# Kernel tuning notes

Measured on AMD Instinct MI355X. Metric: run time of the kernel, lower is better.

## Reference

```python
import jax, jax.numpy as jnp
import numpy as np

NG, NC = 4096, 4096
FIN_G, FIN_C, D = 512, 512, 256
ALPHA = 0.2
NEG = -9.0e15

def leaky(x):
    return jnp.where(x >= 0, x, ALPHA * x)

def setup_inputs() -> dict:
    key = jax.random.key(0)
    ks = jax.random.split(key, 16)
    gene_x = jax.random.normal(ks[0], (NG, FIN_G), jnp.float32)
    cell_x = jax.random.normal(ks[1], (NC, FIN_C), jnp.float32)
    gene_adj = (jax.random.uniform(ks[2], (NG, NG)) < 0.05).astype(jnp.float32)
    gene_adj = jnp.maximum(gene_adj, jnp.eye(NG, dtype=jnp.float32))
    cell_adj = (jax.random.uniform(ks[3], (NC, NC)) < 0.05).astype(jnp.float32)
    cell_adj = jnp.maximum(cell_adj, jnp.eye(NC, dtype=jnp.float32))
    gene_cell_adj = (jax.random.uniform(ks[4], (NG, NC)) < 0.05).astype(jnp.float32)
    s = 1.414 * np.sqrt(6.0)
    def xav(k, shape):
        lim = s / np.sqrt(shape[0] + shape[1])
        return jax.random.uniform(k, shape, jnp.float32, -lim, lim)
    Wg = xav(ks[5], (D, FIN_G))
    Wc = xav(ks[6], (D, FIN_C))
    a_gg = xav(ks[7], (2 * D, 1))
    a_gc = xav(ks[8], (2 * D, 1))
    a_cc = xav(ks[9], (2 * D, 1))
    a_cg = xav(ks[10], (2 * D, 1))
    gate_g_w = xav(ks[11], (1, D))
    gate_c_w = xav(ks[12], (1, D))
    gate_g_b = jnp.full((1,), -2.0, jnp.float32)
    gate_c_b = jnp.full((1,), -2.0, jnp.float32)
    return dict(gene_x=gene_x, cell_x=cell_x, gene_adj=gene_adj, cell_adj=cell_adj,
                gene_cell_adj=gene_cell_adj, Wg=Wg, Wc=Wc, a_gg=a_gg, a_gc=a_gc,
                a_cc=a_cc, a_cg=a_cg, gate_g_w=gate_g_w, gate_g_b=gate_g_b,
                gate_c_w=gate_c_w, gate_c_b=gate_c_b)

def _gat_block(src_h, dst_h, a, adj):
    # attention of src rows over dst columns; adj: [Ns, Nd]
    d = src_h.shape[1]
    s1 = src_h @ a[:d, :]          # [Ns,1]
    s2 = dst_h @ a[d:, :]          # [Nd,1]
    e = leaky(s1 + s2.T)           # [Ns,Nd]
    att = jax.nn.softmax(jnp.where(adj > 0, e, NEG), axis=1)
    return att @ dst_h             # [Ns,d]

def reference(gene_x, cell_x, gene_adj, cell_adj, gene_cell_adj,
              Wg, Wc, a_gg, a_gc, a_cc, a_cg,
              gate_g_w, gate_g_b, gate_c_w, gate_c_b):
    gene_h = gene_x @ Wg.T   # [Ng,D]
    cell_h = cell_x @ Wc.T   # [Nc,D]
    gene_from_gene = _gat_block(gene_h, gene_h, a_gg, gene_adj)
    gene_from_cell = _gat_block(gene_h, cell_h, a_gc, gene_cell_adj)
    cell_from_cell = _gat_block(cell_h, cell_h, a_cc, cell_adj)
    cell_from_gene = _gat_block(cell_h, gene_h, a_cg, gene_cell_adj.T)
    gamma_g = jax.nn.sigmoid(gene_h @ gate_g_w.T + gate_g_b)  # [Ng,1]
    gamma_c = jax.nn.sigmoid(cell_h @ gate_c_w.T + gate_c_b)  # [Nc,1]
    gene_out = leaky(gene_h + gene_from_gene + gamma_g * gene_from_cell)
    cell_out = leaky(cell_h + cell_from_cell + gamma_c * cell_from_gene)
    return gene_out, cell_out
```

## Files before the change

kernel.cpp:

```cpp
#include <hip/hip_runtime.h>
#include <stdint.h>

#define NGC 4096
#define FIN 512
#define DD  256

typedef __attribute__((ext_vector_type(8))) short short8;
typedef __attribute__((ext_vector_type(4))) float f32x4;
typedef unsigned short u16;
typedef unsigned int   u32;
typedef unsigned long long u64;

static __device__ __forceinline__ float bf2f(u16 u){ return __uint_as_float(((u32)u)<<16); }
static __device__ __forceinline__ u16 f2bf(float f){
  u32 u = __float_as_uint(f);
  u += 0x7fffu + ((u>>16)&1u);
  return (u16)(u>>16);
}
static __device__ __forceinline__ float lk(float x){ return fmaxf(x, 0.2f*x); }
static __device__ __forceinline__ u64 shfl_xor64(u64 x, int m){
  u32 lo = (u32)x, hi = (u32)(x >> 32);
  lo = __shfl_xor(lo, m); hi = __shfl_xor(hi, m);
  return ((u64)hi << 32) | lo;
}

__global__ __launch_bounds__(256) void k_wcvt(
    const float* __restrict__ Wg, const float* __restrict__ Wc,
    u16* __restrict__ Wgbf, u16* __restrict__ Wcbf)
{
  int base = (blockIdx.x*256 + threadIdx.x)*4;
  float4 a = *(const float4*)(Wg + base);
  float4 b = *(const float4*)(Wc + base);
  ushort4 oa, ob;
  oa.x=f2bf(a.x); oa.y=f2bf(a.y); oa.z=f2bf(a.z); oa.w=f2bf(a.w);
  ob.x=f2bf(b.x); ob.y=f2bf(b.y); ob.z=f2bf(b.z); ob.w=f2bf(b.w);
  *(ushort4*)(Wgbf + base) = oa;
  *(ushort4*)(Wcbf + base) = ob;
}

__global__ __launch_bounds__(256) void k_pack(
    const float* __restrict__ gene_adj, const float* __restrict__ cell_adj,
    const float* __restrict__ gc_adj,   u64* __restrict__ packbits)
{
  int t = threadIdx.x, wid = t>>6, lane = t&63;
  int gw = blockIdx.x*4 + wid;
  int mat = gw >> 12;
  int row = gw & 4095;
  const float* src = (mat==0) ? gene_adj : (mat==1) ? cell_adj : gc_adj;
  const float* rp = src + (size_t)row*NGC;

  u64 myword = 0;
  #pragma unroll
  for(int i = 0; i < 16; i++){
    float4 v = *(const float4*)(rp + i*256 + lane*4);
    u32 nib = (v.x!=0.f?1u:0u) | (v.y!=0.f?2u:0u) | (v.z!=0.f?4u:0u) | (v.w!=0.f?8u:0u);
    u32 b  = nib | (__shfl_xor((int)nib, 1) << 4);
    u32 h  = b   | (__shfl_xor((int)b,   2) << 8);
    u32 w  = h   | (__shfl_xor((int)h,   4) << 16);
    u32 o  = (u32)__shfl_xor((int)w, 8);
    u32 flo = w, fhi = o;
    int srcl = ((lane - i*4) << 4) & 63;
    u32 glo = (u32)__shfl((int)flo, srcl);
    u32 ghi = (u32)__shfl((int)fhi, srcl);
    if((lane >> 2) == i) myword = ((u64)ghi << 32) | (u64)glo;
  }
  packbits[((size_t)mat << 18) + (size_t)row*64 + lane] = myword;
}

__global__ __launch_bounds__(256) void k_bitTT(
    const u64* __restrict__ gcb, u64* __restrict__ bT)
{
  int t = threadIdx.x, wid = t>>6, lane = t&63;
  int id = blockIdx.x*4 + wid;
  int G = id & 63, C = id >> 6;

  u64 x = gcb[(size_t)(64*G + lane)*64 + C];

  const u64 M1  = 0xAAAAAAAAAAAAAAAAull;
  const u64 M2  = 0xCCCCCCCCCCCCCCCCull;
  const u64 M4  = 0xF0F0F0F0F0F0F0F0ull;
  const u64 M8  = 0xFF00FF00FF00FF00ull;
  const u64 M16 = 0xFFFF0000FFFF0000ull;
  const u64 M32 = 0xFFFFFFFF00000000ull;
  #define TSTEP(S, M) { u64 y = shfl_xor64(x, S); \
    x = (lane & S) ? ((x & (M)) | ((y >> S) & ~(M))) \
                   : ((x & ~(M)) | ((y << S) & (M))); }
  TSTEP(32, M32) TSTEP(16, M16) TSTEP(8, M8)
  TSTEP(4,  M4)  TSTEP(2,  M2)  TSTEP(1, M1)
  #undef TSTEP

  bT[(size_t)(64*C + lane)*64 + G] = x;
}

__global__ __launch_bounds__(512) void k_hgemm(
    const float* __restrict__ xg, const float* __restrict__ xc,
    const u16* __restrict__ Wg, const u16* __restrict__ Wc,
    float* __restrict__ hg, float* __restrict__ hc,
    u16* __restrict__ hTg, u16* __restrict__ hTc)
{
  const int side = blockIdx.y;
  const float* x = side ? xc : xg;
  const u16* W = side ? Wc : Wg;
  float* h  = side ? hc : hg;
  u16*  hT  = side ? hTc : hTg;
  const int r0 = blockIdx.x * 64;
  const int t = threadIdx.x;
  const int wid = t >> 6, lane = t & 63;
  const int lrow = lane & 15, lhi = lane >> 4;

  __shared__ __align__(16) char smem[32768];

  f32x4 acc[4][2];
  const f32x4 z4 = {0.f,0.f,0.f,0.f};
  #pragma unroll
  for(int i=0;i<4;i++){ acc[i][0]=z4; acc[i][1]=z4; }

  const int r = t >> 3, c8 = t & 7;
  for(int k0 = 0; k0 < FIN; k0 += 64){
    const float* xp = x + (size_t)(r0 + r)*FIN + k0 + c8*8;
    float4 xa = *(const float4*)xp;
    float4 xb = *(const float4*)(xp + 4);
    short8 xv;
    xv[0]=(short)f2bf(xa.x); xv[1]=(short)f2bf(xa.y);
    xv[2]=(short)f2bf(xa.z); xv[3]=(short)f2bf(xa.w);
    xv[4]=(short)f2bf(xb.x); xv[5]=(short)f2bf(xb.y);
    xv[6]=(short)f2bf(xb.z); xv[7]=(short)f2bf(xb.w);
    int wbyte = r*128 + (((c8 ^ (r & 7)) & 7) << 4);
    *(short8*)(smem + wbyte) = xv;
    __syncthreads();
    #pragma unroll
    for(int ksub = 0; ksub < 2; ksub++){
      short8 b[2];
      #pragma unroll
      for(int nf=0; nf<2; nf++){
        int n = wid*32 + nf*16 + lrow;
        b[nf] = *(const short8*)(W + (size_t)n*FIN + k0 + ksub*32 + lhi*8);
      }
      #pragma unroll
      for(int mf=0; mf<4; mf++){
        int row = mf*16 + lrow;
        int g = ksub*4 + lhi;
        short8 a = *(const short8*)(smem + row*128 + (((g ^ (row & 7)) & 7) << 4));
        #pragma unroll
        for(int nf=0; nf<2; nf++)
          acc[mf][nf] = __builtin_amdgcn_mfma_f32_16x16x32_bf16(a, b[nf], acc[mf][nf], 0,0,0);
      }
    }
    __syncthreads();
  }
  #pragma unroll
  for(int mf=0; mf<4; mf++){
    #pragma unroll
    for(int nf=0; nf<2; nf++){
      int col = wid*32 + nf*16 + lrow;
      #pragma unroll
      for(int j=0;j<4;j++){
        int row = mf*16 + lhi*4 + j;
        float v = acc[mf][nf][j];
        h[(size_t)(r0+row)*DD + col] = v;
        int byte_ = col*128 + (((row*2) ^ ((col & 7)<<4)));
        *(u16*)(smem + byte_) = f2bf(v);
      }
    }
  }
  __syncthreads();
  {
    int n = t >> 1, half = t & 1;
    #pragma unroll
    for(int gi=0; gi<4; gi++){
      int g = half*4 + gi;
      int byte_ = n*128 + (((g ^ (n & 7)) & 7) << 4);
      short8 v = *(const short8*)(smem + byte_);
      int kcol = r0 + g*8;
      size_t off = (size_t)(kcol>>5)*8192 + (size_t)(n>>4)*512 + (n&15)*32 + (kcol&31);
      *(short8*)(hT + off) = v;
    }
  }
}

__global__ __launch_bounds__(256) void k_svec(
    const float* __restrict__ hg, const float* __restrict__ hc,
    const float* __restrict__ a_gg, const float* __restrict__ a_gc,
    const float* __restrict__ a_cc, const float* __restrict__ a_cg,
    const float* __restrict__ gw_g, const float* __restrict__ gb_g,
    const float* __restrict__ gw_c, const float* __restrict__ gb_c,
    float* __restrict__ sbuf)
{
  int t = threadIdx.x, wid = t>>6, lane = t&63;
  int idx = blockIdx.x * 4 + wid;
  int side = idx >> 12;
  int row  = idx & 4095;
  const float* h = (side ? hc : hg) + (size_t)row*DD;
  const float* v0 = (side ? a_cc : a_gg);
  const float* v1 = (side ? a_cc : a_gg) + DD;
  const float* v2 = (side ? a_cg : a_gc);
  const float* v3 = (side ? a_gc : a_cg) + DD;
  const float* gw = side ? gw_c : gw_g;
  float bias = (side ? gb_c : gb_g)[0];

  float4 hv = *(const float4*)(h + lane*4);
  float4 w0 = *(const float4*)(v0 + lane*4);
  float4 w1 = *(const float4*)(v1 + lane*4);
  float4 w2 = *(const float4*)(v2 + lane*4);
  float4 w3 = *(const float4*)(v3 + lane*4);
  float4 w4 = *(const float4*)(gw + lane*4);

  float d0 = hv.x*w0.x + hv.y*w0.y + hv.z*w0.z + hv.w*w0.w;
  float d1 = hv.x*w1.x + hv.y*w1.y + hv.z*w1.z + hv.w*w1.w;
  float d2 = hv.x*w2.x + hv.y*w2.y + hv.z*w2.z + hv.w*w2.w;
  float d3 = hv.x*w3.x + hv.y*w3.y + hv.z*w3.z + hv.w*w3.w;
  float d4 = hv.x*w4.x + hv.y*w4.y + hv.z*w4.z + hv.w*w4.w;
  #pragma unroll
  for(int s=1;s<64;s<<=1){
    d0 += __shfl_xor(d0, s); d1 += __shfl_xor(d1, s); d2 += __shfl_xor(d2, s);
    d3 += __shfl_xor(d3, s); d4 += __shfl_xor(d4, s);
  }
  if(lane == 0){
    float gam = 1.f/(1.f + __expf(-(d4 + bias)));
    if(side == 0){
      sbuf[0*4096+row]=d0; sbuf[1*4096+row]=d1; sbuf[2*4096+row]=d2;
      sbuf[3*4096+row]=d3; sbuf[4*4096+row]=gam;
    } else {
      sbuf[5*4096+row]=d0; sbuf[6*4096+row]=d1; sbuf[8*4096+row]=d2;
      sbuf[7*4096+row]=d3; sbuf[9*4096+row]=gam;
    }
  }
}

__global__ __launch_bounds__(256,2) void k_gat(
    const float* __restrict__ sbuf,
    const uint8_t* __restrict__ packbits, const uint8_t* __restrict__ bitsT,
    const u16* __restrict__ hTg, const u16* __restrict__ hTc,
    float* __restrict__ part, float* __restrict__ Zpart)
{
  const int mode = blockIdx.z;
  const int kc   = blockIdx.y;
  const int nodebase = blockIdx.x * 64;
  const int kcbase   = kc * 2048;

  const float* s1; const float* s2; const uint8_t* bits; const u16* hT;
  if(mode == 0){ s1 = sbuf;        s2 = sbuf+4096;   bits = packbits;           hT = hTg; }
  else if(mode == 1){ s1 = sbuf+2*4096; s2 = sbuf+7*4096; bits = packbits+4194304; hT = hTc; }
  else if(mode == 2){ s1 = sbuf+5*4096; s2 = sbuf+6*4096; bits = packbits+2097152; hT = hTc; }
  else { s1 = sbuf+8*4096; s2 = sbuf+3*4096; bits = bitsT; hT = hTg; }

  const int t = threadIdx.x, wid = t>>6, lane = t&63, lrow = lane&15, lhi = lane>>4;
  const int kh = wid >> 1;
  const int ng_sub = wid & 1;

  __shared__ __align__(16) char U[32768];
  __shared__ float red[4];
  char*  mask_l = U;
  float* s2_l   = (float*)(U + 17408);

  {
    int row = t>>2, seg = t&3;
    const char* g = (const char*)bits + (size_t)(nodebase+row)*512 + (kcbase>>3) + seg*64;
    char* d = mask_l + row*272 + seg*64;
    #pragma unroll
    for(int i=0;i<4;i++)
      *(ulonglong2*)(d + i*16) = *(const ulonglong2*)(g + i*16);
  }
  {
    const float* g = s2 + kcbase + t*8;
    *(float4*)(s2_l + t*8)     = *(const float4*)(g);
    *(float4*)(s2_l + t*8 + 4) = *(const float4*)(g + 4);
  }
  float mxv = -1e30f;
  #pragma unroll
  for(int i=0;i<4;i++){
    float4 v = *(const float4*)(s2 + t*16 + i*4);
    mxv = fmaxf(mxv, fmaxf(fmaxf(v.x,v.y), fmaxf(v.z,v.w)));
  }
  #pragma unroll
  for(int sh=1; sh<64; sh<<=1) mxv = fmaxf(mxv, __shfl_xor(mxv, sh));
  if(lane==0) red[wid] = mxv;
  __syncthreads();
  const float maxs2 = fmaxf(fmaxf(red[0],red[1]), fmaxf(red[2],red[3]));

  const int wnode = nodebase + ng_sub*32;
  const float L2E = 1.4426950408889634f;
  float c1[2], c2[2], z[2];
  #pragma unroll
  for(int nf=0; nf<2; nf++){
    float s1v = s1[wnode + nf*16 + lrow];
    float m = lk(s1v + maxs2);
    c1[nf] = (s1v - m)*L2E;
    c2[nf] = (0.2f*s1v - m)*L2E;
    z[nf] = 0.f;
  }

  f32x4 acc[16][2];
  const f32x4 zz = {0.f,0.f,0.f,0.f};
  #pragma unroll
  for(int i=0;i<16;i++){ acc[i][0]=zz; acc[i][1]=zz; }

  const u16* pA = hT + (size_t)((kcbase >> 5) + kh*32)*8192 + lrow*32 + lhi*8;
  const u32* pM0 = (const u32*)(mask_l + (ng_sub*32 + lrow)*272) + kh*32;
  const u32* pM1 = (const u32*)(mask_l + (ng_sub*32 + 16 + lrow)*272) + kh*32;
  const float* ps2 = s2_l + kh*1024 + lhi*8;

  for(int s=0; s<32; s++){
    const int kl = s*32;
    float4 sA = *(const float4*)(ps2 + kl);
    float4 sB = *(const float4*)(ps2 + kl + 4);
    float e1[8], e2[8];
    {
      float sv[8] = {sA.x,sA.y,sA.z,sA.w,sB.x,sB.y,sB.z,sB.w};
      #pragma unroll
      for(int j=0;j<8;j++){ e1[j] = sv[j]*L2E; e2[j] = sv[j]*(0.2f*L2E); }
    }
    u32 mw0 = pM0[s], mw1 = pM1[s];
    short8 b[2];
    #pragma unroll
    for(int nf=0; nf<2; nf++){
      u32 mw = nf ? mw1 : mw0;
      u32 w4[4];
      #pragma unroll
      for(int pr=0; pr<4; pr++){
        float bit0 = (float)((mw >> (lhi*8 + 2*pr  )) & 1u);
        float bit1 = (float)((mw >> (lhi*8 + 2*pr+1)) & 1u);
        float p0 = __builtin_amdgcn_exp2f(fmaxf(c1[nf]+e1[2*pr  ], c2[nf]+e2[2*pr  ])) * bit0;
        float p1 = __builtin_amdgcn_exp2f(fmaxf(c1[nf]+e1[2*pr+1], c2[nf]+e2[2*pr+1])) * bit1;
        z[nf] += p0 + p1;
        u32 q0 = __float_as_uint(p0) + 0x8000u;
        u32 q1 = __float_as_uint(p1) + 0x8000u;
        w4[pr] = (q1 & 0xFFFF0000u) | (q0 >> 16);
      }
      union{ u32 u[4]; short8 s8; } cv;
      cv.u[0]=w4[0]; cv.u[1]=w4[1]; cv.u[2]=w4[2]; cv.u[3]=w4[3];
      b[nf] = cv.s8;
    }
    const u16* pAs = pA + (size_t)s*8192;
    #pragma unroll
    for(int mf=0; mf<16; mf++){
      short8 a = *(const short8*)(pAs + mf*512);
      acc[mf][0] = __builtin_amdgcn_mfma_f32_16x16x32_bf16(a, b[0], acc[mf][0], 0,0,0);
      acc[mf][1] = __builtin_amdgcn_mfma_f32_16x16x32_bf16(a, b[1], acc[mf][1], 0,0,0);
    }
  }

  #pragma unroll
  for(int nf=0; nf<2; nf++){
    z[nf] += __shfl_xor(z[nf], 16);
    z[nf] += __shfl_xor(z[nf], 32);
  }
  if(lhi == 0){
    float* zp = Zpart + (size_t)(mode*4 + kc*2 + kh)*4096 + wnode;
    zp[lrow]      = z[0];
    zp[16 + lrow] = z[1];
  }

  __syncthreads();
  float* R = (float*)U;
  float* po = part + ((size_t)(mode*2 + kc) << 20);
  #pragma unroll
  for(int half=0; half<2; half++){
    if(kh == 1){
      #pragma unroll
      for(int mf8=0; mf8<8; mf8++){
        #pragma unroll
        for(int nf=0; nf<2; nf++){
          int r = ng_sub*32 + nf*16 + lrow;
          int byte_ = r*512 + ((mf8*64 + lhi*16) ^ ((r&7)<<4));
          *(f32x4*)((char*)R + byte_) = acc[half*8 + mf8][nf];
        }
      }
    }
    __syncthreads();
    if(kh == 0){
      #pragma unroll
      for(int mf8=0; mf8<8; mf8++){
        #pragma unroll
        for(int nf=0; nf<2; nf++){
          int r = ng_sub*32 + nf*16 + lrow;
          int byte_ = r*512 + ((mf8*64 + lhi*16) ^ ((r&7)<<4));
          f32x4 o = *(const f32x4*)((const char*)R + byte_);
          o = o + acc[half*8 + mf8][nf];
          int node = nodebase + r;
          *(f32x4*)(po + (size_t)node*256 + (half*8+mf8)*16 + lhi*4) = o;
        }
      }
    }
    __syncthreads();
  }
}

__global__ __launch_bounds__(256) void k_epi(
    const float* __restrict__ hg, const float* __restrict__ hc,
    const float* __restrict__ part, const float* __restrict__ Zpart,
    const float* __restrict__ sbuf, float* __restrict__ out)
{
  int idx = blockIdx.x*256 + threadIdx.x;
  int fid = idx*4;
  int side = fid >> 20;
  int l = fid & 1048575;
  int node = l >> 8;
  int modeA = side ? 2 : 0, modeB = side ? 3 : 1;
  const float* h = side ? hc : hg;
  float gam = sbuf[(side ? 9 : 4)*4096 + node];
  float za = Zpart[(size_t)(modeA*4+0)*4096 + node] + Zpart[(size_t)(modeA*4+1)*4096 + node]
           + Zpart[(size_t)(modeA*4+2)*4096 + node] + Zpart[(size_t)(modeA*4+3)*4096 + node];
  float zb = Zpart[(size_t)(modeB*4+0)*4096 + node] + Zpart[(size_t)(modeB*4+1)*4096 + node]
           + Zpart[(size_t)(modeB*4+2)*4096 + node] + Zpart[(size_t)(modeB*4+3)*4096 + node];
  float rza = 1.f / fmaxf(za, 1e-30f);
  float rzb = 1.f / fmaxf(zb, 1e-30f);
  float4 a0 = *(const float4*)(part + ((size_t)(modeA*2  )<<20) + l);
  float4 a1 = *(const float4*)(part + ((size_t)(modeA*2+1)<<20) + l);
  float4 b0 = *(const float4*)(part + ((size_t)(modeB*2  )<<20) + l);
  float4 b1 = *(const float4*)(part + ((size_t)(modeB*2+1)<<20) + l);
  float4 h4 = *(const float4*)(h + l);
  float4 o;
  o.x = lk(h4.x + (a0.x+a1.x)*rza + gam*(b0.x+b1.x)*rzb);
  o.y = lk(h4.y + (a0.y+a1.y)*rza + gam*(b0.y+b1.y)*rzb);
  o.z = lk(h4.z + (a0.z+a1.z)*rza + gam*(b0.z+b1.z)*rzb);
  o.w = lk(h4.w + (a0.w+a1.w)*rza + gam*(b0.w+b1.w)*rzb);
  *(float4*)(out + fid) = o;
}

extern "C" void kernel_launch(void* const* d_in, const int* in_sizes, int n_in,
                              void* d_out, int out_size, void* d_ws, size_t ws_size,
                              hipStream_t stream)
{
  const float* gene_x   = (const float*)d_in[0];
  const float* cell_x   = (const float*)d_in[1];
  const float* gene_adj = (const float*)d_in[2];
  const float* cell_adj = (const float*)d_in[3];
  const float* gc_adj   = (const float*)d_in[4];
  const float* Wg       = (const float*)d_in[5];
  const float* Wc       = (const float*)d_in[6];
  const float* a_gg     = (const float*)d_in[7];
  const float* a_gc     = (const float*)d_in[8];
  const float* a_cc     = (const float*)d_in[9];
  const float* a_cg     = (const float*)d_in[10];
  const float* gw_g     = (const float*)d_in[11];
  const float* gb_g     = (const float*)d_in[12];
  const float* gw_c     = (const float*)d_in[13];
  const float* gb_c     = (const float*)d_in[14];

  char* ws = (char*)d_ws;
  float* hg   = (float*)(ws);
  float* hc   = (float*)(ws + (4u<<20));
  u16*   hTg  = (u16*)  (ws + (8u<<20));
  u16*   hTc  = (u16*)  (ws + (10u<<20));
  float* sbuf = (float*)(ws + (12u<<20));
  float* Zpart= (float*)(ws + (12u<<20) + (512u<<10));
  uint8_t* bitsT = (uint8_t*)(ws + (13u<<20));
  u16*   Wgbf = (u16*)  (ws + (17u<<20));
  u16*   Wcbf = (u16*)  (ws + (17u<<20) + (512u<<10));
  float* part = (float*)(ws + (17u<<20));
  u64*   packbits = (u64*)(ws + (49u<<20));

  k_wcvt<<<dim3(128), 256, 0, stream>>>(Wg, Wc, Wgbf, Wcbf);
  k_pack<<<dim3(3072), 256, 0, stream>>>(gene_adj, cell_adj, gc_adj, packbits);
  k_bitTT<<<dim3(1024), 256, 0, stream>>>(packbits + 524288, (u64*)bitsT);
  k_hgemm<<<dim3(64,2), 512, 0, stream>>>(gene_x, cell_x, Wgbf, Wcbf, hg, hc, hTg, hTc);
  k_svec<<<dim3(2048), 256, 0, stream>>>(hg, hc, a_gg, a_gc, a_cc, a_cg,
                                         gw_g, gb_g, gw_c, gb_c, sbuf);
  k_gat<<<dim3(64,2,4), 256, 0, stream>>>(sbuf, (const uint8_t*)packbits,
                                          bitsT, hTg, hTc, part, Zpart);
  k_epi<<<dim3(2048), 256, 0, stream>>>(hg, hc, part, Zpart, sbuf, (float*)d_out);
}
```

Measured before the change: 162.6 us.

## Double-buffer hT tiles into LDS via async global_load_lds in attention kernel

The attention-aggregation kernel now stages each 32-wide K slice of the transposed bf16 features into LDS with asynchronous global_load_lds, double-buffered so the next slice loads while MFMAs run on the current one. The hT layout written by the projection kernel is permuted so each lane's 16-byte fragment is contiguous and matches the LDS copy. The mask tile is XOR-swizzled in LDS, and s2 values are prefetched from global into registers instead of staged in shared memory. The cost is 80KB of LDS per block, which lowers occupancy, plus a __syncthreads per iteration.

```diff
diff --git a/kernel.cpp b/kernel.cpp
--- a/kernel.cpp
+++ b/kernel.cpp
@@ -22,6 +22,11 @@
   u32 lo = (u32)x, hi = (u32)(x >> 32);
   lo = __shfl_xor(lo, m); hi = __shfl_xor(hi, m);
   return ((u64)hi << 32) | lo;
+}
+static __device__ __forceinline__ void gl16(const void* g, void* l){
+  __builtin_amdgcn_global_load_lds(
+    (const __attribute__((address_space(1))) void*)g,
+    (__attribute__((address_space(3))) void*)l, 16, 0, 0);
 }
 
 __global__ __launch_bounds__(256) void k_wcvt(
@@ -172,7 +177,8 @@
       int byte_ = n*128 + (((g ^ (n & 7)) & 7) << 4);
       short8 v = *(const short8*)(smem + byte_);
       int kcol = r0 + g*8;
-      size_t off = (size_t)(kcol>>5)*8192 + (size_t)(n>>4)*512 + (n&15)*32 + (kcol&31);
+      size_t off = (size_t)(kcol>>5)*8192 + (size_t)(n>>4)*512
+                 + ((kcol>>3)&3)*128 + (n&15)*8;
       *(short8*)(hT + off) = v;
     }
   }
@@ -248,35 +254,36 @@
   const int kh = wid >> 1;
   const int ng_sub = wid & 1;
 
-  __shared__ __align__(16) char U[32768];
-  __shared__ float red[4];
-  char*  mask_l = U;
-  float* s2_l   = (float*)(U + 17408);
+  __shared__ __align__(16) char U[81920];
+  char* A_lds  = U;
+  char* mask_l = U + 65536;
 
   {
     int row = t>>2, seg = t&3;
-    const char* g = (const char*)bits + (size_t)(nodebase+row)*512 + (kcbase>>3) + seg*64;
-    char* d = mask_l + row*272 + seg*64;
-    #pragma unroll
-    for(int i=0;i<4;i++)
-      *(ulonglong2*)(d + i*16) = *(const ulonglong2*)(g + i*16);
-  }
+    const char* g = (const char*)bits + (size_t)(nodebase+row)*512 + kc*256 + seg*64;
+    char* drow_ = mask_l + row*256;
+    #pragma unroll
+    for(int i=0;i<4;i++){
+      int slot = seg*4 + i;
+      *(ulonglong2*)(drow_ + (((slot ^ (row&7)))<<4)) = *(const ulonglong2*)(g + i*16);
+    }
+  }
+  const char* hTb = (const char*)hT;
   {
-    const float* g = s2 + kcbase + t*8;
-    *(float4*)(s2_l + t*8)     = *(const float4*)(g);
-    *(float4*)(s2_l + t*8 + 4) = *(const float4*)(g + 4);
+    const char* g = hTb + ((size_t)kc*64 + kh*32 + 0)*16384 + ng_sub*8192 + lane*16;
+    char* l = A_lds + 0*32768 + kh*16384 + ng_sub*8192;
+    #pragma unroll
+    for(int i=0;i<8;i++) gl16(g + i*1024, l + i*1024);
   }
   float mxv = -1e30f;
   #pragma unroll
-  for(int i=0;i<4;i++){
-    float4 v = *(const float4*)(s2 + t*16 + i*4);
+  for(int i=0;i<16;i++){
+    float4 v = *(const float4*)(s2 + lane*64 + i*4);
     mxv = fmaxf(mxv, fmaxf(fmaxf(v.x,v.y), fmaxf(v.z,v.w)));
   }
   #pragma unroll
   for(int sh=1; sh<64; sh<<=1) mxv = fmaxf(mxv, __shfl_xor(mxv, sh));
-  if(lane==0) red[wid] = mxv;
-  __syncthreads();
-  const float maxs2 = fmaxf(fmaxf(red[0],red[1]), fmaxf(red[2],red[3]));
+  const float maxs2 = mxv;
 
   const int wnode = nodebase + ng_sub*32;
   const float L2E = 1.4426950408889634f;
@@ -295,22 +302,39 @@
   #pragma unroll
   for(int i=0;i<16;i++){ acc[i][0]=zz; acc[i][1]=zz; }
 
-  const u16* pA = hT + (size_t)((kcbase >> 5) + kh*32)*8192 + lrow*32 + lhi*8;
-  const u32* pM0 = (const u32*)(mask_l + (ng_sub*32 + lrow)*272) + kh*32;
-  const u32* pM1 = (const u32*)(mask_l + (ng_sub*32 + 16 + lrow)*272) + kh*32;
-  const float* ps2 = s2_l + kh*1024 + lhi*8;
-
+  const float* s2g = s2 + kcbase + kh*1024 + lhi*8;
+  const char* mrow0 = mask_l + (ng_sub*32 + lrow)*256;
+  const char* mrow1 = mask_l + (ng_sub*32 + 16 + lrow)*256;
+  const int mx0 = (ng_sub*32 + lrow) & 7, mx1 = (ng_sub*32 + 16 + lrow) & 7;
+
+  float4 csA = *(const float4*)(s2g);
+  float4 csB = *(const float4*)(s2g + 4);
+
+  __syncthreads();
+
+  #pragma unroll 1
   for(int s=0; s<32; s++){
-    const int kl = s*32;
-    float4 sA = *(const float4*)(ps2 + kl);
-    float4 sB = *(const float4*)(ps2 + kl + 4);
+    const int cur = s & 1;
+    if(s < 31){
+      const char* g = hTb + ((size_t)kc*64 + kh*32 + s + 1)*16384 + ng_sub*8192 + lane*16;
+      char* l = A_lds + (cur^1)*32768 + kh*16384 + ng_sub*8192;
+      #pragma unroll
+      for(int i=0;i<8;i++) gl16(g + i*1024, l + i*1024);
+    }
+    float4 sA = csA, sB = csB;
+    if(s < 31){
+      csA = *(const float4*)(s2g + (s+1)*32);
+      csB = *(const float4*)(s2g + (s+1)*32 + 4);
+    }
     float e1[8], e2[8];
     {
       float sv[8] = {sA.x,sA.y,sA.z,sA.w,sB.x,sB.y,sB.z,sB.w};
       #pragma unroll
       for(int j=0;j<8;j++){ e1[j] = sv[j]*L2E; e2[j] = sv[j]*(0.2f*L2E); }
     }
-    u32 mw0 = pM0[s], mw1 = pM1[s];
+    const int slot = kh*8 + (s>>2), win = (s&3)*4;
+    u32 mw0 = *(const u32*)(mrow0 + ((slot ^ mx0)<<4) + win);
+    u32 mw1 = *(const u32*)(mrow1 + ((slot ^ mx1)<<4) + win);
     short8 b[2];
     #pragma unroll
     for(int nf=0; nf<2; nf++){
@@ -331,13 +355,14 @@
       cv.u[0]=w4[0]; cv.u[1]=w4[1]; cv.u[2]=w4[2]; cv.u[3]=w4[3];
       b[nf] = cv.s8;
     }
-    const u16* pAs = pA + (size_t)s*8192;
+    const char* Af = A_lds + cur*32768 + kh*16384 + lane*16;
     #pragma unroll
     for(int mf=0; mf<16; mf++){
-      short8 a = *(const short8*)(pAs + mf*512);
+      short8 a = *(const short8*)(Af + mf*1024);
       acc[mf][0] = __builtin_amdgcn_mfma_f32_16x16x32_bf16(a, b[0], acc[mf][0], 0,0,0);
       acc[mf][1] = __builtin_amdgcn_mfma_f32_16x16x32_bf16(a, b[1], acc[mf][1], 0,0,0);
     }
+    __syncthreads();
   }
 
   #pragma unroll
@@ -352,7 +377,7 @@
   }
 
   __syncthreads();
-  float* R = (float*)U;
+  float* R = (float*)A_lds;
   float* po = part + ((size_t)(mode*2 + kc) << 20);
   #pragma unroll
   for(int half=0; half<2; half++){
```

New measurement: 136.2 us. -16.2%, faster.
